# Kernel optimization log

Hardware: AMD Instinct MI355X
Metric: run time of the kernel (lower is better)

Reference implementation:

```python
import jax, jax.numpy as jnp
import numpy as np

N_FEATURES = 256  # channels; vectors have sizes 2..256 (255 vectors)
EPS = 1e-16


def _pad_mask(m, n):
    # row i holds a vector of size i+2, right-aligned; left part is constant 1-padding
    return jnp.arange(n)[None, :] >= (n - 2 - jnp.arange(m))[:, None]


def setup_inputs() -> dict:
    key = jax.random.key(0)
    k1, k2, k3 = jax.random.split(key, 3)
    B, C, H, W = 32, N_FEATURES, 64, 64
    x = jax.random.normal(k1, (B, C, H, W), dtype=jnp.float32)
    log_det_jac = jnp.zeros((B,), dtype=jnp.float32)
    z = jax.random.normal(k2, (B, 16), dtype=jnp.float32)
    V = jax.random.normal(k3, (C - 1, C), dtype=jnp.float32)
    # mimic reset_parameters: each vector scaled to unit norm (over its real entries)
    mask = _pad_mask(C - 1, C)
    norms = jnp.sqrt(jnp.sum(jnp.where(mask, V, 0.0) ** 2, axis=1, keepdims=True)) + EPS
    V = V / norms
    return {"x": x, "log_det_jac": log_det_jac, "z": z, "V": V}


def _cascade(V, n):
    # Q <- Q @ (I - 2 v v^T / (v.v + eps)) applied sequentially == rank-1 update
    mask = _pad_mask(V.shape[0], n)
    Vfull = jnp.where(mask, V, 1.0)  # prepend ones like householder_matrix

    def step(Q, v):
        inner = jnp.dot(v, v) + EPS
        Qv = Q @ v  # [n]
        return Q - (2.0 / inner) * jnp.outer(Qv, v), None

    Q0 = jnp.eye(n, dtype=V.dtype)
    Q, _ = jax.lax.scan(step, Q0, Vfull)
    return Q


def reference(x, log_det_jac, z, V):
    W = _cascade(V, N_FEATURES)  # [C, C] orthogonal
    # 1x1 conv: y[b,o,h,w] = sum_c W[o,c] x[b,c,h,w]
    y = jnp.einsum('oc,bchw->bohw', W, x)
    return y, log_det_jac + 0.0, z
```

## Files before the change

kernel.cpp:

```cpp
#include <hip/hip_runtime.h>
#include <stdint.h>

typedef __attribute__((ext_vector_type(8))) short short8v;
typedef __attribute__((ext_vector_type(4))) float f32x4;

__device__ __forceinline__ unsigned short f2bf(float f) {
  union { float f; unsigned int i; } v; v.f = f;
  unsigned int x = v.i;
  x += 0x7FFFu + ((x >> 16) & 1u);
  return (unsigned short)(x >> 16);
}

__global__ void __launch_bounds__(256) prep_kernel(const float* __restrict__ V,
                                                   float* __restrict__ Vs,
                                                   const float* __restrict__ ldj,
                                                   const float* __restrict__ z,
                                                   float* __restrict__ out) {
  const int k = blockIdx.x;
  const int c = threadIdx.x;
  if (k == 255) {
    if (c < 32) out[33554432u + c] = ldj[c];
    out[33554464u + c] = z[c];
    out[33554464u + 256u + c] = z[256u + c];
    return;
  }
  float val = (c >= 254 - k) ? V[k * 256 + c] : 1.0f;
  float ss = val * val;
  #pragma unroll
  for (int off = 32; off >= 1; off >>= 1) ss += __shfl_xor(ss, off);
  __shared__ float part[4];
  if ((threadIdx.x & 63) == 0) part[threadIdx.x >> 6] = ss;
  __syncthreads();
  const float tot = part[0] + part[1] + part[2] + part[3];
  const float s = sqrtf(2.0f / (tot + 1e-16f));
  Vs[k * 256 + c] = s * val;
}

__global__ void __launch_bounds__(256) cascade_kernel(const float* __restrict__ Vs,
                                                      unsigned short* __restrict__ Wb) {
  const int w = threadIdx.x >> 6;
  const int l = threadIdx.x & 63;
  const int r0 = blockIdx.x * 16 + w * 4;

  f32x4 q[4];
  #pragma unroll
  for (int j = 0; j < 4; ++j) {
    const int r = r0 + j;
    q[j][0] = (4 * l + 0 == r) ? 1.0f : 0.0f;
    q[j][1] = (4 * l + 1 == r) ? 1.0f : 0.0f;
    q[j][2] = (4 * l + 2 == r) ? 1.0f : 0.0f;
    q[j][3] = (4 * l + 3 == r) ? 1.0f : 0.0f;
  }

  const f32x4* __restrict__ Vs4 = (const f32x4*)Vs;
  f32x4 vn = Vs4[l];
  for (int k = 0; k < 255; ++k) {
    const f32x4 v = vn;
    if (k + 1 < 255) vn = Vs4[(k + 1) * 64 + l];
    float p[4];
    #pragma unroll
    for (int j = 0; j < 4; ++j)
      p[j] = q[j][0] * v[0] + q[j][1] * v[1] + q[j][2] * v[2] + q[j][3] * v[3];
    #pragma unroll
    for (int off = 32; off >= 1; off >>= 1) {
      #pragma unroll
      for (int j = 0; j < 4; ++j) p[j] += __shfl_xor(p[j], off);
    }
    #pragma unroll
    for (int j = 0; j < 4; ++j) {
      q[j][0] -= p[j] * v[0];
      q[j][1] -= p[j] * v[1];
      q[j][2] -= p[j] * v[2];
      q[j][3] -= p[j] * v[3];
    }
  }

  #pragma unroll
  for (int j = 0; j < 4; ++j) {
    ushort4 o;
    o.x = f2bf(q[j][0]); o.y = f2bf(q[j][1]); o.z = f2bf(q[j][2]); o.w = f2bf(q[j][3]);
    *(ushort4*)(Wb + (size_t)(r0 + j) * 256 + 4 * l) = o;
  }
}

__global__ void __launch_bounds__(512) conv_kernel(const float* __restrict__ x,
                                                   const unsigned short* __restrict__ Wb,
                                                   float* __restrict__ y) {
  __shared__ unsigned int lds[2048];

  const int b  = blockIdx.y;
  const int n0 = blockIdx.x * 64;
  const int t  = threadIdx.x;
  const int w  = t >> 6;
  const int l  = t & 63;
  const int lr = l & 15;
  const int lg = l >> 4;
  const int nq = t & 15;
  const int kb = t >> 4;

  const float* __restrict__ xb = x + (size_t)b * (256u * 4096u);
  float* __restrict__ yb = y + (size_t)b * (256u * 4096u);

  f32x4 acc[2][4];
  #pragma unroll
  for (int i = 0; i < 2; ++i)
    #pragma unroll
    for (int j = 0; j < 4; ++j)
      acc[i][j] = (f32x4){0.f, 0.f, 0.f, 0.f};

  f32x4 r0, r1;
  {
    const f32x4* p = (const f32x4*)(xb + (size_t)(2 * kb) * 4096 + n0) + nq;
    r0 = p[0];
    r1 = p[1024];
  }

  for (int T = 0; T < 4; ++T) {
    unsigned int packed[4];
    #pragma unroll
    for (int j = 0; j < 4; ++j)
      packed[j] = (unsigned int)f2bf(r0[j]) | ((unsigned int)f2bf(r1[j]) << 16);

    if (T) __syncthreads();
    #pragma unroll
    for (int jj = 0; jj < 4; ++jj) {
      const int j = (jj + nq) & 3;
      const int n = 4 * nq + j;
      const int dw = n * 32 + ((((kb >> 2) ^ (n & 7)) << 2) | (kb & 3));
      lds[dw] = packed[j];
    }
    __syncthreads();

    if (T < 3) {
      const f32x4* p = (const f32x4*)(xb + (size_t)(64 * (T + 1) + 2 * kb) * 4096 + n0) + nq;
      r0 = p[0];
      r1 = p[1024];
    }

    #pragma unroll
    for (int s = 0; s < 2; ++s) {
      short8v a[2], bb[4];
      #pragma unroll
      for (int i = 0; i < 2; ++i)
        a[i] = *(const short8v*)(Wb + (size_t)(32 * w + 16 * i + lr) * 256
                                 + 64 * T + 32 * s + 8 * lg);
      #pragma unroll
      for (int jn = 0; jn < 4; ++jn) {
        const int n = 16 * jn + lr;
        const int dw = n * 32 + ((((s << 2) + lg) ^ (lr & 7)) << 2);
        bb[jn] = *(const short8v*)(&lds[dw]);
      }
      #pragma unroll
      for (int i = 0; i < 2; ++i)
        #pragma unroll
        for (int jn = 0; jn < 4; ++jn)
          acc[i][jn] = __builtin_amdgcn_mfma_f32_16x16x32_bf16(a[i], bb[jn], acc[i][jn], 0, 0, 0);
    }
  }

  #pragma unroll
  for (int i = 0; i < 2; ++i)
    #pragma unroll
    for (int jn = 0; jn < 4; ++jn)
      #pragma unroll
      for (int rr = 0; rr < 4; ++rr) {
        const int o = 32 * w + 16 * i + 4 * lg + rr;
        yb[(size_t)o * 4096 + n0 + 16 * jn + lr] = acc[i][jn][rr];
      }
}

extern "C" void kernel_launch(void* const* d_in, const int* in_sizes, int n_in,
                              void* d_out, int out_size, void* d_ws, size_t ws_size,
                              hipStream_t stream) {
  const float* x   = (const float*)d_in[0];
  const float* ldj = (const float*)d_in[1];
  const float* z   = (const float*)d_in[2];
  const float* V   = (const float*)d_in[3];
  float* out = (float*)d_out;

  float* Vs = (float*)d_ws;
  unsigned short* Wb = (unsigned short*)((char*)d_ws + 1048576);

  prep_kernel<<<256, 256, 0, stream>>>(V, Vs, ldj, z, out);
  cascade_kernel<<<16, 256, 0, stream>>>(Vs, Wb);
  dim3 grid(64, 32);
  conv_kernel<<<grid, 512, 0, stream>>>(x, Wb, out);
}
```

Measured before the change: 154.1 us.

## Replace serial Householder cascade with blocked compact-WY products

```diff
diff --git a/kernel.cpp b/kernel.cpp
--- a/kernel.cpp
+++ b/kernel.cpp
@@ -10,6 +10,16 @@
   x += 0x7FFFu + ((x >> 16) & 1u);
   return (unsigned short)(x >> 16);
 }
+
+#define WSF_VS 0
+#define WSF_SS 65536
+#define WSF_A  81920
+#define OF_P0T 0
+#define OF_P1  65536
+#define OF_P2T 131072
+#define OF_P3  196608
+#define OF_P01T 262144
+#define OF_P23  327680
 
 __global__ void __launch_bounds__(256) prep_kernel(const float* __restrict__ V,
                                                    float* __restrict__ Vs,
@@ -18,12 +28,13 @@
                                                    float* __restrict__ out) {
   const int k = blockIdx.x;
   const int c = threadIdx.x;
-  if (k == 255) {
+  if (k == 256) {
     if (c < 32) out[33554432u + c] = ldj[c];
     out[33554464u + c] = z[c];
     out[33554464u + 256u + c] = z[256u + c];
     return;
   }
+  if (k == 255) { Vs[255 * 256 + c] = 0.0f; return; }
   float val = (c >= 254 - k) ? V[k * 256 + c] : 1.0f;
   float ss = val * val;
   #pragma unroll
@@ -36,51 +47,112 @@
   Vs[k * 256 + c] = s * val;
 }
 
-__global__ void __launch_bounds__(256) cascade_kernel(const float* __restrict__ Vs,
-                                                      unsigned short* __restrict__ Wb) {
-  const int w = threadIdx.x >> 6;
-  const int l = threadIdx.x & 63;
-  const int r0 = blockIdx.x * 16 + w * 4;
-
-  f32x4 q[4];
-  #pragma unroll
-  for (int j = 0; j < 4; ++j) {
-    const int r = r0 + j;
-    q[j][0] = (4 * l + 0 == r) ? 1.0f : 0.0f;
-    q[j][1] = (4 * l + 1 == r) ? 1.0f : 0.0f;
-    q[j][2] = (4 * l + 2 == r) ? 1.0f : 0.0f;
-    q[j][3] = (4 * l + 3 == r) ? 1.0f : 0.0f;
-  }
-
-  const f32x4* __restrict__ Vs4 = (const f32x4*)Vs;
-  f32x4 vn = Vs4[l];
-  for (int k = 0; k < 255; ++k) {
-    const f32x4 v = vn;
-    if (k + 1 < 255) vn = Vs4[(k + 1) * 64 + l];
-    float p[4];
-    #pragma unroll
-    for (int j = 0; j < 4; ++j)
-      p[j] = q[j][0] * v[0] + q[j][1] * v[1] + q[j][2] * v[2] + q[j][3] * v[3];
-    #pragma unroll
-    for (int off = 32; off >= 1; off >>= 1) {
-      #pragma unroll
-      for (int j = 0; j < 4; ++j) p[j] += __shfl_xor(p[j], off);
-    }
-    #pragma unroll
-    for (int j = 0; j < 4; ++j) {
-      q[j][0] -= p[j] * v[0];
-      q[j][1] -= p[j] * v[1];
-      q[j][2] -= p[j] * v[2];
-      q[j][3] -= p[j] * v[3];
-    }
-  }
-
-  #pragma unroll
-  for (int j = 0; j < 4; ++j) {
-    ushort4 o;
-    o.x = f2bf(q[j][0]); o.y = f2bf(q[j][1]); o.z = f2bf(q[j][2]); o.w = f2bf(q[j][3]);
-    *(ushort4*)(Wb + (size_t)(r0 + j) * 256 + 4 * l) = o;
-  }
+__global__ void __launch_bounds__(256) gram_kernel(const float* __restrict__ Vs,
+                                                   float* __restrict__ SS) {
+  const int g = blockIdx.y, is = blockIdx.x;
+  const int w = threadIdx.x >> 6, j = threadIdx.x & 63;
+  #pragma unroll
+  for (int ii = 0; ii < 2; ++ii) {
+    const int i = is * 8 + w * 2 + ii;
+    if (i < j) {
+      const f32x4* vi = (const f32x4*)(Vs + (size_t)(g * 64 + i) * 256);
+      const f32x4* vj = (const f32x4*)(Vs + (size_t)(g * 64 + j) * 256);
+      f32x4 acc = {0.f, 0.f, 0.f, 0.f};
+      #pragma unroll
+      for (int q = 0; q < 64; ++q) {
+        const f32x4 a = vi[q], b = vj[q];
+        acc[0] += a[0] * b[0]; acc[1] += a[1] * b[1];
+        acc[2] += a[2] * b[2]; acc[3] += a[3] * b[3];
+      }
+      SS[(g * 64 + j) * 64 + i] = (acc[0] + acc[1]) + (acc[2] + acc[3]);
+    }
+  }
+}
+
+__global__ void __launch_bounds__(256) solve_kernel(const float* __restrict__ Vs,
+                                                    const float* __restrict__ SS,
+                                                    float* __restrict__ A) {
+  const int g = blockIdx.x, d = threadIdx.x;
+  const float* Vg = Vs + (size_t)g * 64 * 256;
+  const float* Sg = SS + g * 64 * 64;
+  float a[64];
+  a[0] = Vg[d];
+  #pragma unroll
+  for (int j = 1; j < 64; ++j) {
+    float s0 = 0.f, s1 = 0.f, s2 = 0.f, s3 = 0.f;
+    #pragma unroll
+    for (int i = 0; i < 64; i += 4) {
+      if (i + 0 < j) s0 += Sg[j * 64 + i + 0] * a[i + 0];
+      if (i + 1 < j) s1 += Sg[j * 64 + i + 1] * a[i + 1];
+      if (i + 2 < j) s2 += Sg[j * 64 + i + 2] * a[i + 2];
+      if (i + 3 < j) s3 += Sg[j * 64 + i + 3] * a[i + 3];
+    }
+    a[j] = Vg[j * 256 + d] - ((s0 + s1) + (s2 + s3));
+  }
+  #pragma unroll
+  for (int j = 0; j < 64; ++j) A[(size_t)(g * 64 + j) * 256 + d] = a[j];
+}
+
+__global__ void __launch_bounds__(256) formp_kernel(const float* __restrict__ Vs,
+                                                    const float* __restrict__ A,
+                                                    float* __restrict__ outF) {
+  const int rt = blockIdx.x, g = blockIdx.y;
+  const int c = threadIdx.x;
+  const bool tr = ((g & 1) == 0);
+  const float* uni = (tr ? Vs : A) + (size_t)g * 64 * 256;
+  const float* coa = (tr ? A : Vs) + (size_t)g * 64 * 256;
+  float* Pg = outF + (size_t)g * 65536;
+  float acc[64];
+  #pragma unroll
+  for (int r = 0; r < 64; ++r) acc[r] = (rt * 64 + r == c) ? 1.0f : 0.0f;
+  for (int j = 0; j < 64; ++j) {
+    const float v = coa[j * 256 + c];
+    const float* ur = uni + j * 256 + rt * 64;
+    #pragma unroll
+    for (int r = 0; r < 64; ++r) acc[r] -= ur[r] * v;
+  }
+  #pragma unroll
+  for (int r = 0; r < 64; ++r) Pg[(size_t)(rt * 64 + r) * 256 + c] = acc[r];
+}
+
+__global__ void __launch_bounds__(256) mulpair_kernel(float* __restrict__ outF) {
+  const int ct = blockIdx.x, rt = blockIdx.y, z = blockIdx.z;
+  const float* XT = outF + (z == 0 ? OF_P1 : OF_P2T);
+  const float* Y  = outF + (z == 0 ? OF_P0T : OF_P3);
+  float* Z        = outF + (z == 0 ? OF_P01T : OF_P23);
+  const int c  = ct * 64 + (threadIdx.x & 63);
+  const int r0 = rt * 64 + (threadIdx.x >> 6) * 16;
+  float acc[16];
+  #pragma unroll
+  for (int q = 0; q < 16; ++q) acc[q] = 0.f;
+  for (int k = 0; k < 256; ++k) {
+    const float yv = Y[k * 256 + c];
+    const float* xr = XT + k * 256 + r0;
+    #pragma unroll
+    for (int q = 0; q < 16; ++q) acc[q] += xr[q] * yv;
+  }
+  #pragma unroll
+  for (int q = 0; q < 16; ++q) Z[(size_t)(r0 + q) * 256 + c] = acc[q];
+}
+
+__global__ void __launch_bounds__(256) mulfinal_kernel(const float* __restrict__ outF,
+                                                       unsigned short* __restrict__ Wb) {
+  const int ct = blockIdx.x, rt = blockIdx.y;
+  const float* XT = outF + OF_P01T;
+  const float* Y  = outF + OF_P23;
+  const int c  = ct * 64 + (threadIdx.x & 63);
+  const int r0 = rt * 64 + (threadIdx.x >> 6) * 16;
+  float acc[16];
+  #pragma unroll
+  for (int q = 0; q < 16; ++q) acc[q] = 0.f;
+  for (int k = 0; k < 256; ++k) {
+    const float yv = Y[k * 256 + c];
+    const float* xr = XT + k * 256 + r0;
+    #pragma unroll
+    for (int q = 0; q < 16; ++q) acc[q] += xr[q] * yv;
+  }
+  #pragma unroll
+  for (int q = 0; q < 16; ++q) Wb[(size_t)(r0 + q) * 256 + c] = f2bf(acc[q]);
 }
 
 __global__ void __launch_bounds__(512) conv_kernel(const float* __restrict__ x,
@@ -178,11 +250,18 @@
   const float* V   = (const float*)d_in[3];
   float* out = (float*)d_out;
 
-  float* Vs = (float*)d_ws;
-  unsigned short* Wb = (unsigned short*)((char*)d_ws + 1048576);
-
-  prep_kernel<<<256, 256, 0, stream>>>(V, Vs, ldj, z, out);
-  cascade_kernel<<<16, 256, 0, stream>>>(Vs, Wb);
+  float* wsF = (float*)d_ws;
+  float* Vs = wsF + WSF_VS;
+  float* SS = wsF + WSF_SS;
+  float* A  = wsF + WSF_A;
+  unsigned short* Wb = (unsigned short*)((char*)d_ws + (size_t)(WSF_A + 65536) * 4);
+
+  prep_kernel<<<257, 256, 0, stream>>>(V, Vs, ldj, z, out);
+  gram_kernel<<<dim3(8, 4), 256, 0, stream>>>(Vs, SS);
+  solve_kernel<<<4, 256, 0, stream>>>(Vs, SS, A);
+  formp_kernel<<<dim3(4, 4), 256, 0, stream>>>(Vs, A, out);
+  mulpair_kernel<<<dim3(4, 4, 2), 256, 0, stream>>>(out);
+  mulfinal_kernel<<<dim3(4, 4), 256, 0, stream>>>(out, Wb);
   dim3 grid(64, 32);
   conv_kernel<<<grid, 512, 0, stream>>>(x, Wb, out);
 }
```

New measurement: 372.6 us. +141.8%, slower.
